# Optimization experiments

Hardware: AMD Instinct MI355X
Metric: run time of the kernel (lower is better)

The kernel has to match this reference:

```python
import jax, jax.numpy as jnp
import numpy as np
from jax.scipy.special import gammaln

B, T, U = 65536, 64, 8


def gamma_filter(tau, n, T):
    # tau, n: (1, U) already mulFac-scaled. Matches generate_simple_filter_multichan.
    t = jnp.arange(T, dtype=jnp.float32)[:, None]            # (T, 1)
    f = t ** n * jnp.exp(-t / tau)                           # (T, U); f[0]=0 since n>0
    f = f / (tau ** (n + 1.0)) / jnp.exp(gammaln(n + 1.0))
    return f                                                 # (T, U)


def causal_conv(x, K):
    # x: (B, T), K: (T, U). y[b,t,u] = sum_{j<=t} x[b,t-j] * K[j,u]
    # == tf.nn.conv2d with reversed kernel and causal left-pad (T-1, 0).
    T = x.shape[1]
    idx = jnp.arange(T)[:, None] - jnp.arange(T)[None, :]    # (T, T) = t - t'
    Kmat = jnp.where(idx[:, :, None] >= 0, K[jnp.clip(idx, 0, T - 1)], 0.0)  # (T, T, U)
    return jnp.einsum('bs,tsu->btu', x, Kmat)                # (B, T, U)


def setup_inputs() -> dict:
    key = jax.random.key(0)
    ks = jax.random.split(key, 12)
    uni = lambda k, lo, hi: jax.random.uniform(k, (1, U), minval=lo, maxval=hi, dtype=jnp.float32)
    return {
        'inputs': jax.random.uniform(ks[0], (B, T, 1), dtype=jnp.float32),  # light intensity >= 0
        'alpha': uni(ks[1], 0.001, 0.1),
        'beta':  uni(ks[2], 0.001, 0.1),
        'gamma': uni(ks[3], 0.01, 0.1),
        'zeta':  uni(ks[4], 0.0, 0.1),      # computed but unused by call()
        'tauY':  uni(ks[5], 0.001, 0.02),   # y-path is dead code (unused by outputs)
        'nY':    uni(ks[6], 1e-5, 0.1),
        'tauZ':  uni(ks[7], 0.3, 1.0),
        'nZ':    jnp.full((1, U), 0.01, jnp.float32),  # frozen constant in the layer
        'tauC':  uni(ks[8], 0.01, 0.5),
        'nC':    jnp.full((1, U), 0.01, jnp.float32),  # frozen constant in the layer
    }


def reference(inputs, alpha, beta, gamma, zeta, tauY, nY, tauZ, nZ, tauC, nC):
    Bv, Tv, P = inputs.shape  # P == 1 (pixels folded into batch)
    a = alpha * 100.0         # alpha_mulFac
    b = beta * 10.0           # beta_mulFac
    g = gamma * 10.0          # gamma_mulFac
    tau_z = tauZ * 100.0
    n_z = nZ * 10.0
    tau_c = tauC * 100.0
    n_c = nC * 10.0

    Kc = gamma_filter(tau_c, n_c, Tv)                      # (T, U)
    Kz = g[0][None, :] * Kc + (1.0 - g[0][None, :]) * gamma_filter(tau_z, n_z, Tv)

    x = inputs[:, :, 0]                                    # (B, T)
    z = causal_conv(x, Kz)                                 # (B, T, U)

    # slice_tensor: per-unit gather at flat time index (T - argmax_t Kz)
    z_shift = jnp.argmax(Kz, axis=0)                       # (U,), >=1 since Kz[0]=0
    t_idx = jnp.clip(Tv - z_shift, 0, Tv - 1)
    z_sel = z[:, t_idx, jnp.arange(U)]                     # (B, U)

    # outputs = alpha * x / (1 + beta * z), broadcast to (B, T, 1, 1, U)
    out = (a[0][None, None, None, None, :] * inputs[:, :, :, None, None]
           / (1.0 + b[0][None, None, None, None, :] * z_sel[:, None, None, None, :]))
    return out
```

## Files before the change

### kernel.cpp

```cpp
#include <hip/hip_runtime.h>
#include <math.h>

#define TSZ 64
#define USZ 8
#define NB  16
#define XS  68

typedef float nfloat4 __attribute__((ext_vector_type(4)));


__global__ __launch_bounds__(1024) void setup_kernel(const float* __restrict__ alpha,
                             const float* __restrict__ beta,
                             const float* __restrict__ gamma_,
                             const float* __restrict__ tauZ,
                             const float* __restrict__ nZ,
                             const float* __restrict__ tauC,
                             const float* __restrict__ nC,
                             float* __restrict__ ws) {
    __shared__ float kbuf[2][USZ][TSZ];
    __shared__ float kz[USZ][TSZ];
    __shared__ int ti_s[USZ];

    const int tid = threadIdx.x;
    {
        const int fid = tid >> 9;
        const int rem = tid & 511;
        const int u   = rem >> 6;
        const int t   = rem & 63;
        const float tf = (float)t;
        float tau, n;
        if (fid == 0) { tau = tauC[u] * 100.0f; n = nC[u] * 10.0f; }
        else          { tau = tauZ[u] * 100.0f; n = nZ[u] * 10.0f; }
        float f = powf(tf, n) * expf(-tf / tau) / powf(tau, n + 1.0f) / tgammaf(n + 1.0f);
        kbuf[fid][u][t] = f;
    }
    __syncthreads();
    if (tid < 512) {
        const int u = tid >> 6;
        const int t = tid & 63;
        float g = gamma_[u] * 10.0f;
        kz[u][t] = g * kbuf[0][u][t] + (1.0f - g) * kbuf[1][u][t];
    }
    __syncthreads();
    if (tid < USZ) {
        const int u = tid;
        float best = kz[u][0];
        int bi = 0;
        for (int s = 1; s < TSZ; ++s) {
            float v = kz[u][s];
            if (v > best) { best = v; bi = s; }
        }
        int ti = TSZ - bi;
        if (ti > TSZ - 1) ti = TSZ - 1;
        if (ti < 0) ti = 0;
        ti_s[u] = ti;
        ws[512 + u] = alpha[u] * 100.0f;
        ws[520 + u] = beta[u]  * 10.0f;
    }
    __syncthreads();
    if (tid < 512) {
        const int u = tid >> 6;
        const int t = tid & 63;
        int ti = ti_s[u];
        ws[u * TSZ + t] = (t <= ti) ? kz[u][ti - t] : 0.0f;
    }
}

__global__ __launch_bounds__(256) void main_kernel(const float* __restrict__ x,
                                                   const float* __restrict__ ws,
                                                   float* __restrict__ out) {
    __shared__ __attribute__((aligned(16))) float xs[NB * XS];
    __shared__ __attribute__((aligned(16))) float wl[USZ * XS];
    __shared__ __attribute__((aligned(16))) float fs[NB * USZ];

    const int tid = threadIdx.x;
    const int blk = blockIdx.x;

    if (tid < 128) {
        float4 v = ((const float4*)ws)[tid];
        int u  = tid >> 4;
        int s0 = (tid & 15) << 2;
        *((float4*)&wl[u * XS + s0]) = v;
    }
    {
        const float4* x4 = (const float4*)(x + (size_t)blk * NB * TSZ);
        float4 v = x4[tid];
        int bl = tid >> 4;
        int s0 = (tid & 15) << 2;
        *((float4*)&xs[bl * XS + s0]) = v;
    }
    __syncthreads();

    if (tid < NB * USZ) {
        const int bl = tid >> 3;
        const int u  = tid & 7;
        const float4* xr = (const float4*)&xs[bl * XS];
        const float4* wr = (const float4*)&wl[u * XS];
        float acc = 0.0f;
        #pragma unroll
        for (int j = 0; j < 16; ++j) {
            float4 a = xr[j];
            float4 b = wr[j];
            acc += a.x * b.x + a.y * b.y + a.z * b.z + a.w * b.w;
        }
        float av = ws[512 + u];
        float bv = ws[520 + u];
        fs[bl * USZ + u] = av / (1.0f + bv * acc);
    }
    __syncthreads();

    nfloat4* o4 = (nfloat4*)(out + (size_t)blk * NB * TSZ * USZ);
    #pragma unroll
    for (int k = 0; k < 8; ++k) {
        int j = tid + k * 256;
        int bl   = j >> 7;
        int r    = j & 127;
        int t    = r >> 1;
        int half = r & 1;
        float xv = xs[bl * XS + t];
        float4 f = *((const float4*)&fs[bl * USZ + half * 4]);
        nfloat4 o;
        o.x = xv * f.x; o.y = xv * f.y; o.z = xv * f.z; o.w = xv * f.w;
        __builtin_nontemporal_store(o, &o4[j]);
    }
}

extern "C" void kernel_launch(void* const* d_in, const int* in_sizes, int n_in,
                              void* d_out, int out_size, void* d_ws, size_t ws_size,
                              hipStream_t stream) {
    const float* inputs = (const float*)d_in[0];
    const float* alpha  = (const float*)d_in[1];
    const float* beta   = (const float*)d_in[2];
    const float* gamma_ = (const float*)d_in[3];
    const float* tauZ   = (const float*)d_in[7];
    const float* nZ     = (const float*)d_in[8];
    const float* tauC   = (const float*)d_in[9];
    const float* nC     = (const float*)d_in[10];
    float* out = (float*)d_out;
    float* ws  = (float*)d_ws;

    setup_kernel<<<1, 1024, 0, stream>>>(alpha, beta, gamma_, tauZ, nZ, tauC, nC, ws);

    const int B = in_sizes[0] / TSZ;
    main_kernel<<<B / NB, 256, 0, stream>>>(inputs, ws, out);
}
```

Measured before the change: 173.3 us.

## Use one wavefront per batch row with shuffle reductions and a persistent grid

```diff
diff --git a/kernel.cpp b/kernel.cpp
--- a/kernel.cpp
+++ b/kernel.cpp
@@ -3,10 +3,6 @@
 
 #define TSZ 64
 #define USZ 8
-#define NB  16
-#define XS  68
-
-typedef float nfloat4 __attribute__((ext_vector_type(4)));
 
 
 __global__ __launch_bounds__(1024) void setup_kernel(const float* __restrict__ alpha,
@@ -68,60 +64,45 @@
 
 __global__ __launch_bounds__(256) void main_kernel(const float* __restrict__ x,
                                                    const float* __restrict__ ws,
-                                                   float* __restrict__ out) {
-    __shared__ __attribute__((aligned(16))) float xs[NB * XS];
-    __shared__ __attribute__((aligned(16))) float wl[USZ * XS];
-    __shared__ __attribute__((aligned(16))) float fs[NB * USZ];
+                                                   float* __restrict__ out,
+                                                   int nbatch) {
+    const int lane = threadIdx.x & 63;
+    const int wid  = (blockIdx.x << 2) | (threadIdx.x >> 6);
+    const int nwaves = gridDim.x << 2;
 
-    const int tid = threadIdx.x;
-    const int blk = blockIdx.x;
+    float wreg[USZ], av[USZ], bv[USZ];
+    #pragma unroll
+    for (int u = 0; u < USZ; ++u) {
+        wreg[u] = ws[u * TSZ + lane];
+        av[u]   = ws[512 + u];
+        bv[u]   = ws[520 + u];
+    }
 
-    if (tid < 128) {
-        float4 v = ((const float4*)ws)[tid];
-        int u  = tid >> 4;
-        int s0 = (tid & 15) << 2;
-        *((float4*)&wl[u * XS + s0]) = v;
-    }
-    {
-        const float4* x4 = (const float4*)(x + (size_t)blk * NB * TSZ);
-        float4 v = x4[tid];
-        int bl = tid >> 4;
-        int s0 = (tid & 15) << 2;
-        *((float4*)&xs[bl * XS + s0]) = v;
-    }
-    __syncthreads();
+    int b = wid;
+    float xv = x[(size_t)b * TSZ + lane];
+    for (; b < nbatch; ) {
+        int bn = b + nwaves;
+        float xn = 0.0f;
+        if (bn < nbatch) xn = x[(size_t)bn * TSZ + lane];
 
-    if (tid < NB * USZ) {
-        const int bl = tid >> 3;
-        const int u  = tid & 7;
-        const float4* xr = (const float4*)&xs[bl * XS];
-        const float4* wr = (const float4*)&wl[u * XS];
-        float acc = 0.0f;
+        float f[USZ];
         #pragma unroll
-        for (int j = 0; j < 16; ++j) {
-            float4 a = xr[j];
-            float4 b = wr[j];
-            acc += a.x * b.x + a.y * b.y + a.z * b.z + a.w * b.w;
+        for (int u = 0; u < USZ; ++u) {
+            float p = xv * wreg[u];
+            #pragma unroll
+            for (int m = 1; m < 64; m <<= 1) p += __shfl_xor(p, m);
+            f[u] = av[u] / (1.0f + bv[u] * p);
         }
-        float av = ws[512 + u];
-        float bv = ws[520 + u];
-        fs[bl * USZ + u] = av / (1.0f + bv * acc);
-    }
-    __syncthreads();
 
-    nfloat4* o4 = (nfloat4*)(out + (size_t)blk * NB * TSZ * USZ);
-    #pragma unroll
-    for (int k = 0; k < 8; ++k) {
-        int j = tid + k * 256;
-        int bl   = j >> 7;
-        int r    = j & 127;
-        int t    = r >> 1;
-        int half = r & 1;
-        float xv = xs[bl * XS + t];
-        float4 f = *((const float4*)&fs[bl * USZ + half * 4]);
-        nfloat4 o;
-        o.x = xv * f.x; o.y = xv * f.y; o.z = xv * f.z; o.w = xv * f.w;
-        __builtin_nontemporal_store(o, &o4[j]);
+        float4* o4 = (float4*)(out + (size_t)b * (TSZ * USZ) + lane * USZ);
+        float4 lo, hi;
+        lo.x = xv * f[0]; lo.y = xv * f[1]; lo.z = xv * f[2]; lo.w = xv * f[3];
+        hi.x = xv * f[4]; hi.y = xv * f[5]; hi.z = xv * f[6]; hi.w = xv * f[7];
+        o4[0] = lo;
+        o4[1] = hi;
+
+        b = bn;
+        xv = xn;
     }
 }
 
@@ -141,6 +122,6 @@
 
     setup_kernel<<<1, 1024, 0, stream>>>(alpha, beta, gamma_, tauZ, nZ, tauC, nC, ws);
 
-    const int B = in_sizes[0] / TSZ;
-    main_kernel<<<B / NB, 256, 0, stream>>>(inputs, ws, out);
+    const int nbatch = in_sizes[0] / TSZ;
+    main_kernel<<<2048, 256, 0, stream>>>(inputs, ws, out, nbatch);
 }
```

Measured after the change: 184.2 us. 6.3% more time.
